# Optimization experiments

Hardware: AMD Instinct MI355X
Metric: run time of the kernel (lower is better)

The kernel has to match this reference:

```python
import jax, jax.numpy as jnp
import numpy as np

N_NODES = 50000
N_EDGES = 800000
IN_CH = 128
OUT_CH = 64
BN_EPS = 1e-5


def setup_inputs() -> dict:
    key = jax.random.key(0)
    k1, k2, k3 = jax.random.split(key, 3)
    x = jax.random.normal(k1, (N_NODES, IN_CH), dtype=jnp.float32)
    edge_index = jax.random.randint(k2, (2, N_EDGES), 0, N_NODES, dtype=jnp.int64)
    W = jax.random.normal(k3, (IN_CH, OUT_CH), dtype=jnp.float32) / np.sqrt(IN_CH)
    bias = jnp.zeros((OUT_CH,), dtype=jnp.float32)
    gamma = jnp.ones((OUT_CH,), dtype=jnp.float32)
    beta = jnp.zeros((OUT_CH,), dtype=jnp.float32)
    return {"x": x, "edge_index": edge_index, "W": W, "bias": bias,
            "gamma": gamma, "beta": beta}


def reference(x, edge_index, W, bias, gamma, beta):
    N = x.shape[0]
    # Linear transform first (GCNConv order): [N, out]
    h = x @ W
    # Add self-loops
    loops = jnp.arange(N, dtype=edge_index.dtype)
    src = jnp.concatenate([edge_index[0], loops])  # [E+N]
    dst = jnp.concatenate([edge_index[1], loops])
    # Symmetric GCN normalization: deg^{-1/2}[src] * deg^{-1/2}[dst]
    ones = jnp.ones(dst.shape[0], dtype=h.dtype)
    deg = jax.ops.segment_sum(ones, dst, num_segments=N)
    dinv = jnp.where(deg > 0, jax.lax.rsqrt(deg), 0.0)
    norm = dinv[src] * dinv[dst]  # [E+N]
    # Gather, scale, scatter-add
    msgs = h[src] * norm[:, None]  # [E+N, out]
    agg = jax.ops.segment_sum(msgs, dst, num_segments=N) + bias  # [N, out]
    # tanh activation
    a = jnp.tanh(agg)
    # BatchNorm over node dim (training mode, biased var)
    mean = jnp.mean(a, axis=0)
    var = jnp.mean(jnp.square(a - mean), axis=0)
    return gamma * (a - mean) * jax.lax.rsqrt(var + BN_EPS) + beta
```

## Files before the change

kernel.cpp:

```cpp
#include <hip/hip_runtime.h>
#include <hip/hip_bf16.h>
#include <math.h>

#define N_NODES 50000
#define N_EDGES 800000
#define IN_CH 128
#define OUT_CH 64
#define BN_EPS 1e-5f
#define CAP 64

typedef __attribute__((ext_vector_type(8))) short short8;
typedef __attribute__((ext_vector_type(4))) float f32x4;

__device__ __forceinline__ float bf16u_to_f32(uint u) { return __uint_as_float(u << 16); }

__device__ __forceinline__ ushort f32_to_bf16(float f) {
    uint u = __float_as_uint(f);
    uint r = (u + 0x7fff + ((u >> 16) & 1)) >> 16;
    return (ushort)r;
}

__global__ void fill_slots_kernel(const int4* __restrict__ esrc4, const int4* __restrict__ edst4,
                                  int* __restrict__ cnt, ushort* __restrict__ slot, int E4) {
    int i = blockIdx.x * blockDim.x + threadIdx.x;
    if (i < E4) {
        int4 s = esrc4[i];
        int4 d = edst4[i];
        int p;
        p = atomicAdd(&cnt[d.x], 1); if (p < CAP) slot[d.x * CAP + p] = (ushort)s.x;
        p = atomicAdd(&cnt[d.y], 1); if (p < CAP) slot[d.y * CAP + p] = (ushort)s.y;
        p = atomicAdd(&cnt[d.z], 1); if (p < CAP) slot[d.z * CAP + p] = (ushort)s.z;
        p = atomicAdd(&cnt[d.w], 1); if (p < CAP) slot[d.w * CAP + p] = (ushort)s.w;
    }
}

__global__ void prep_kernel(const int* __restrict__ cnt, float* __restrict__ dinv,
                            float* __restrict__ sums, int N) {
    int i = blockIdx.x * blockDim.x + threadIdx.x;
    if (i < N) dinv[i] = rsqrtf((float)(cnt[i] + 1));
    if (i < 128) sums[i] = 0.0f;
}

#define XPAD 136
__global__ __launch_bounds__(256) void gemm_mfma_kernel(const float* __restrict__ x,
                                                        const float* __restrict__ W,
                                                        ushort* __restrict__ hb, int N) {
    __shared__ ushort xs[64 * XPAD];
    __shared__ ushort wt[64 * XPAD];
    int t = threadIdx.x;
    int lane = t & 63;
    int w = t >> 6;
    int nn = lane & 15;
    int quad = lane >> 4;
    int row0 = blockIdx.x * 64;

#pragma unroll
    for (int i = 0; i < 32; ++i) {
        int wlin = t + 256 * i;
        int k = wlin >> 6, n = wlin & 63;
        wt[n * XPAD + k] = f32_to_bf16(W[wlin]);
    }
#pragma unroll
    for (int i = 0; i < 8; ++i) {
        int linear4 = t + 256 * i;
        int r = linear4 >> 5;
        int c4 = linear4 & 31;
        int gr = row0 + r; if (gr >= N) gr = N - 1;
        float4 v = *(const float4*)(x + (size_t)gr * IN_CH + c4 * 4);
        ushort u0 = f32_to_bf16(v.x), u1 = f32_to_bf16(v.y);
        ushort u2 = f32_to_bf16(v.z), u3 = f32_to_bf16(v.w);
        uint2 packed = make_uint2((uint)u0 | ((uint)u1 << 16), (uint)u2 | ((uint)u3 << 16));
        *(uint2*)&xs[r * XPAD + c4 * 4] = packed;
    }
    __syncthreads();

    short8 bfrag[4][4];
#pragma unroll
    for (int t2 = 0; t2 < 4; ++t2)
#pragma unroll
        for (int c = 0; c < 4; ++c)
            bfrag[t2][c] = *(const short8*)&wt[(16 * t2 + nn) * XPAD + 32 * c + quad * 8];

    f32x4 acc[4] = {{0.f, 0.f, 0.f, 0.f}, {0.f, 0.f, 0.f, 0.f},
                    {0.f, 0.f, 0.f, 0.f}, {0.f, 0.f, 0.f, 0.f}};
#pragma unroll
    for (int c = 0; c < 4; ++c) {
        short8 afrag = *(const short8*)&xs[(16 * w + nn) * XPAD + 32 * c + quad * 8];
#pragma unroll
        for (int t2 = 0; t2 < 4; ++t2)
            acc[t2] = __builtin_amdgcn_mfma_f32_16x16x32_bf16(afrag, bfrag[t2][c], acc[t2], 0, 0, 0);
    }

#pragma unroll
    for (int t2 = 0; t2 < 4; ++t2) {
#pragma unroll
        for (int r = 0; r < 4; ++r) {
            int row = row0 + 16 * w + quad * 4 + r;
            if (row < N) hb[(size_t)row * OUT_CH + 16 * t2 + nn] = f32_to_bf16(acc[t2][r]);
        }
    }
}

__global__ __launch_bounds__(256) void gather_fused_kernel(const int* __restrict__ cnt,
                                                           const ushort* __restrict__ slot,
                                                           const float* __restrict__ dinv,
                                                           const ushort* __restrict__ hb,
                                                           const float* __restrict__ bias,
                                                           float* __restrict__ out,
                                                           float* __restrict__ sums, int N) {
    int t = threadIdx.x;
    int lane = t & 63;
    int wid = (blockIdx.x * blockDim.x + t) >> 6;
    int nw = (gridDim.x * blockDim.x) >> 6;
    float bias_c = bias[lane];
    float ssum = 0.f, ssq = 0.f;

    for (int d = wid; d < N; d += nw) {
        float dd = dinv[d];
        float acc = bf16u_to_f32(hb[(size_t)d * OUT_CH + lane]) * dd * dd;
        int m = cnt[d]; if (m > CAP) m = CAP;
        int sv = __builtin_nontemporal_load(&slot[(size_t)d * CAP + lane]);
        if (lane >= m) sv = 0;
        float dv = dinv[sv];
        int j = 0;
        for (; j + 3 < m; j += 4) {
            int s0 = __shfl(sv, j + 0); float w0 = __shfl(dv, j + 0);
            int s1 = __shfl(sv, j + 1); float w1 = __shfl(dv, j + 1);
            int s2 = __shfl(sv, j + 2); float w2 = __shfl(dv, j + 2);
            int s3 = __shfl(sv, j + 3); float w3 = __shfl(dv, j + 3);
            uint h0 = hb[(size_t)s0 * OUT_CH + lane];
            uint h1 = hb[(size_t)s1 * OUT_CH + lane];
            uint h2 = hb[(size_t)s2 * OUT_CH + lane];
            uint h3 = hb[(size_t)s3 * OUT_CH + lane];
            acc += bf16u_to_f32(h0) * (w0 * dd);
            acc += bf16u_to_f32(h1) * (w1 * dd);
            acc += bf16u_to_f32(h2) * (w2 * dd);
            acc += bf16u_to_f32(h3) * (w3 * dd);
        }
        for (; j < m; ++j) {
            int s = __shfl(sv, j);
            float ww = __shfl(dv, j) * dd;
            acc += bf16u_to_f32(hb[(size_t)s * OUT_CH + lane]) * ww;
        }
        float v = tanhf(acc + bias_c);
        out[(size_t)d * OUT_CH + lane] = v;
        ssum += v;
        ssq += v * v;
    }

    __shared__ float ls[256];
    __shared__ float ls2[256];
    ls[t] = ssum; ls2[t] = ssq;
    __syncthreads();
    if (t < 128) { ls[t] += ls[t + 128]; ls2[t] += ls2[t + 128]; }
    __syncthreads();
    if (t < 64) {
        atomicAdd(&sums[t], ls[t] + ls[t + 64]);
        atomicAdd(&sums[64 + t], ls2[t] + ls2[t + 64]);
    }
}

__global__ __launch_bounds__(256) void bn_apply_kernel(float4* __restrict__ a,
                                                       const float* __restrict__ sums,
                                                       const float* __restrict__ gamma,
                                                       const float* __restrict__ beta, int total4) {
    int c0 = (threadIdx.x * 4) & 63;
    const float invN = 1.0f / (float)N_NODES;
    float4 scale, shift;
    {
        float m0 = sums[c0 + 0] * invN, m1 = sums[c0 + 1] * invN;
        float m2 = sums[c0 + 2] * invN, m3 = sums[c0 + 3] * invN;
        float v0 = sums[64 + c0 + 0] * invN - m0 * m0;
        float v1 = sums[64 + c0 + 1] * invN - m1 * m1;
        float v2 = sums[64 + c0 + 2] * invN - m2 * m2;
        float v3 = sums[64 + c0 + 3] * invN - m3 * m3;
        scale.x = gamma[c0 + 0] * rsqrtf(v0 + BN_EPS);
        scale.y = gamma[c0 + 1] * rsqrtf(v1 + BN_EPS);
        scale.z = gamma[c0 + 2] * rsqrtf(v2 + BN_EPS);
        scale.w = gamma[c0 + 3] * rsqrtf(v3 + BN_EPS);
        shift.x = beta[c0 + 0] - m0 * scale.x;
        shift.y = beta[c0 + 1] - m1 * scale.y;
        shift.z = beta[c0 + 2] - m2 * scale.z;
        shift.w = beta[c0 + 3] - m3 * scale.w;
    }
    int stride = gridDim.x * blockDim.x;
    for (int idx = blockIdx.x * blockDim.x + threadIdx.x; idx < total4; idx += stride) {
        float4 v = a[idx];
        v.x = v.x * scale.x + shift.x;
        v.y = v.y * scale.y + shift.y;
        v.z = v.z * scale.z + shift.z;
        v.w = v.w * scale.w + shift.w;
        a[idx] = v;
    }
}

extern "C" void kernel_launch(void* const* d_in, const int* in_sizes, int n_in,
                              void* d_out, int out_size, void* d_ws, size_t ws_size,
                              hipStream_t stream) {
    const float* x     = (const float*)d_in[0];
    const int*   eidx  = (const int*)d_in[1];
    const float* W     = (const float*)d_in[2];
    const float* bias  = (const float*)d_in[3];
    const float* gamma = (const float*)d_in[4];
    const float* beta  = (const float*)d_in[5];
    float* out = (float*)d_out;

    const int4* esrc4 = (const int4*)eidx;
    const int4* edst4 = (const int4*)(eidx + N_EDGES);

    ushort* hb   = (ushort*)d_ws;
    int*   cnt   = (int*)(hb + (size_t)N_NODES * OUT_CH);
    float* sums  = (float*)(cnt + N_NODES);
    float* dinv  = sums + 128;
    ushort* slot = (ushort*)(dinv + N_NODES);

    hipMemsetAsync(cnt, 0, (size_t)N_NODES * 4, stream);
    fill_slots_kernel<<<(N_EDGES / 4 + 255) / 256, 256, 0, stream>>>(esrc4, edst4, cnt, slot, N_EDGES / 4);
    prep_kernel<<<(N_NODES + 255) / 256, 256, 0, stream>>>(cnt, dinv, sums, N_NODES);
    gemm_mfma_kernel<<<(N_NODES + 63) / 64, 256, 0, stream>>>(x, W, hb, N_NODES);
    gather_fused_kernel<<<2048, 256, 0, stream>>>(cnt, slot, dinv, hb, bias, out, sums, N_NODES);
    bn_apply_kernel<<<512, 256, 0, stream>>>((float4*)out, sums, gamma, beta, N_NODES * OUT_CH / 4);
}
```

Baseline: 234.4 us.

## Replace fixed-capacity slot adjacency with compact count-scan-fill CSR buckets

```diff
diff --git a/kernel.cpp b/kernel.cpp
--- a/kernel.cpp
+++ b/kernel.cpp
@@ -7,7 +7,8 @@
 #define IN_CH 128
 #define OUT_CH 64
 #define BN_EPS 1e-5f
-#define CAP 64
+#define GB 782
+#define CB 782
 
 typedef __attribute__((ext_vector_type(8))) short short8;
 typedef __attribute__((ext_vector_type(4))) float f32x4;
@@ -20,34 +21,29 @@
     return (ushort)r;
 }
 
-__global__ void fill_slots_kernel(const int4* __restrict__ esrc4, const int4* __restrict__ edst4,
-                                  int* __restrict__ cnt, ushort* __restrict__ slot, int E4) {
-    int i = blockIdx.x * blockDim.x + threadIdx.x;
-    if (i < E4) {
-        int4 s = esrc4[i];
-        int4 d = edst4[i];
-        int p;
-        p = atomicAdd(&cnt[d.x], 1); if (p < CAP) slot[d.x * CAP + p] = (ushort)s.x;
-        p = atomicAdd(&cnt[d.y], 1); if (p < CAP) slot[d.y * CAP + p] = (ushort)s.y;
-        p = atomicAdd(&cnt[d.z], 1); if (p < CAP) slot[d.z * CAP + p] = (ushort)s.z;
-        p = atomicAdd(&cnt[d.w], 1); if (p < CAP) slot[d.w * CAP + p] = (ushort)s.w;
-    }
-}
-
-__global__ void prep_kernel(const int* __restrict__ cnt, float* __restrict__ dinv,
-                            float* __restrict__ sums, int N) {
-    int i = blockIdx.x * blockDim.x + threadIdx.x;
-    if (i < N) dinv[i] = rsqrtf((float)(cnt[i] + 1));
-    if (i < 128) sums[i] = 0.0f;
-}
-
 #define XPAD 136
-__global__ __launch_bounds__(256) void gemm_mfma_kernel(const float* __restrict__ x,
-                                                        const float* __restrict__ W,
-                                                        ushort* __restrict__ hb, int N) {
+
+__global__ __launch_bounds__(256) void gemm_count_kernel(const float* __restrict__ x,
+                                                         const float* __restrict__ W,
+                                                         ushort* __restrict__ hb,
+                                                         const int4* __restrict__ edst4,
+                                                         int* __restrict__ cnt, int N, int E4) {
     __shared__ ushort xs[64 * XPAD];
     __shared__ ushort wt[64 * XPAD];
     int t = threadIdx.x;
+
+    if (blockIdx.x >= GB) {
+        int i = (blockIdx.x - GB) * 256 + t;
+        if (i < E4) {
+            int4 d = edst4[i];
+            atomicAdd(&cnt[d.x], 1);
+            atomicAdd(&cnt[d.y], 1);
+            atomicAdd(&cnt[d.z], 1);
+            atomicAdd(&cnt[d.w], 1);
+        }
+        return;
+    }
+
     int lane = t & 63;
     int w = t >> 6;
     int nn = lane & 15;
@@ -101,8 +97,53 @@
     }
 }
 
+__global__ __launch_bounds__(256) void alloc_kernel(const int* __restrict__ cnt,
+                                                    int* __restrict__ gcur,
+                                                    int* __restrict__ offsets,
+                                                    int* __restrict__ cursor,
+                                                    float* __restrict__ dinv,
+                                                    float* __restrict__ sums, int N) {
+    __shared__ int ls[256];
+    __shared__ int sbase;
+    int t = threadIdx.x;
+    int i = blockIdx.x * 256 + t;
+    int c = (i < N) ? cnt[i] : 0;
+    ls[t] = c;
+    __syncthreads();
+    for (int off = 1; off < 256; off <<= 1) {
+        int u = (t >= off) ? ls[t - off] : 0;
+        __syncthreads();
+        ls[t] += u;
+        __syncthreads();
+    }
+    if (t == 255) sbase = atomicAdd(gcur, ls[255]);
+    __syncthreads();
+    if (i < N) {
+        int excl = ls[t] - c + sbase;
+        offsets[i] = excl;
+        cursor[i] = excl;
+        dinv[i] = rsqrtf((float)(c + 1));
+    }
+    if (blockIdx.x == 0 && t < 128) sums[t] = 0.0f;
+}
+
+__global__ void fill_kernel(const int4* __restrict__ esrc4, const int4* __restrict__ edst4,
+                            int* __restrict__ cursor, ushort* __restrict__ bucket, int E4) {
+    int i = blockIdx.x * blockDim.x + threadIdx.x;
+    if (i < E4) {
+        int4 s = esrc4[i];
+        int4 d = edst4[i];
+        int p;
+        p = atomicAdd(&cursor[d.x], 1); bucket[p] = (ushort)s.x;
+        p = atomicAdd(&cursor[d.y], 1); bucket[p] = (ushort)s.y;
+        p = atomicAdd(&cursor[d.z], 1); bucket[p] = (ushort)s.z;
+        p = atomicAdd(&cursor[d.w], 1); bucket[p] = (ushort)s.w;
+    }
+}
+
 __global__ __launch_bounds__(256) void gather_fused_kernel(const int* __restrict__ cnt,
-                                                           const ushort* __restrict__ slot,
+                                                           const int* __restrict__ offsets,
+                                                           const ushort* __restrict__ bucket,
                                                            const float* __restrict__ dinv,
                                                            const ushort* __restrict__ hb,
                                                            const float* __restrict__ bias,
@@ -118,29 +159,36 @@
     for (int d = wid; d < N; d += nw) {
         float dd = dinv[d];
         float acc = bf16u_to_f32(hb[(size_t)d * OUT_CH + lane]) * dd * dd;
-        int m = cnt[d]; if (m > CAP) m = CAP;
-        int sv = __builtin_nontemporal_load(&slot[(size_t)d * CAP + lane]);
-        if (lane >= m) sv = 0;
-        float dv = dinv[sv];
-        int j = 0;
-        for (; j + 3 < m; j += 4) {
-            int s0 = __shfl(sv, j + 0); float w0 = __shfl(dv, j + 0);
-            int s1 = __shfl(sv, j + 1); float w1 = __shfl(dv, j + 1);
-            int s2 = __shfl(sv, j + 2); float w2 = __shfl(dv, j + 2);
-            int s3 = __shfl(sv, j + 3); float w3 = __shfl(dv, j + 3);
-            uint h0 = hb[(size_t)s0 * OUT_CH + lane];
-            uint h1 = hb[(size_t)s1 * OUT_CH + lane];
-            uint h2 = hb[(size_t)s2 * OUT_CH + lane];
-            uint h3 = hb[(size_t)s3 * OUT_CH + lane];
-            acc += bf16u_to_f32(h0) * (w0 * dd);
-            acc += bf16u_to_f32(h1) * (w1 * dd);
-            acc += bf16u_to_f32(h2) * (w2 * dd);
-            acc += bf16u_to_f32(h3) * (w3 * dd);
-        }
-        for (; j < m; ++j) {
-            int s = __shfl(sv, j);
-            float ww = __shfl(dv, j) * dd;
-            acc += bf16u_to_f32(hb[(size_t)s * OUT_CH + lane]) * ww;
+        int b0 = offsets[d];
+        int b1 = b0 + cnt[d];
+        for (int base = b0; base < b1; base += 64) {
+            int idx = base + lane;
+            int sv = 0; float dv = 0.f;
+            if (idx < b1) {
+                sv = __builtin_nontemporal_load(&bucket[idx]);
+                dv = dinv[sv];
+            }
+            int m = b1 - base; if (m > 64) m = 64;
+            int j = 0;
+            for (; j + 3 < m; j += 4) {
+                int s0 = __shfl(sv, j + 0); float w0 = __shfl(dv, j + 0);
+                int s1 = __shfl(sv, j + 1); float w1 = __shfl(dv, j + 1);
+                int s2 = __shfl(sv, j + 2); float w2 = __shfl(dv, j + 2);
+                int s3 = __shfl(sv, j + 3); float w3 = __shfl(dv, j + 3);
+                uint h0 = hb[(size_t)s0 * OUT_CH + lane];
+                uint h1 = hb[(size_t)s1 * OUT_CH + lane];
+                uint h2 = hb[(size_t)s2 * OUT_CH + lane];
+                uint h3 = hb[(size_t)s3 * OUT_CH + lane];
+                acc += bf16u_to_f32(h0) * (w0 * dd);
+                acc += bf16u_to_f32(h1) * (w1 * dd);
+                acc += bf16u_to_f32(h2) * (w2 * dd);
+                acc += bf16u_to_f32(h3) * (w3 * dd);
+            }
+            for (; j < m; ++j) {
+                int s = __shfl(sv, j);
+                float ww = __shfl(dv, j) * dd;
+                acc += bf16u_to_f32(hb[(size_t)s * OUT_CH + lane]) * ww;
+            }
         }
         float v = tanhf(acc + bias_c);
         out[(size_t)d * OUT_CH + lane] = v;
@@ -207,17 +255,21 @@
 
     const int4* esrc4 = (const int4*)eidx;
     const int4* edst4 = (const int4*)(eidx + N_EDGES);
-
-    ushort* hb   = (ushort*)d_ws;
-    int*   cnt   = (int*)(hb + (size_t)N_NODES * OUT_CH);
-    float* sums  = (float*)(cnt + N_NODES);
-    float* dinv  = sums + 128;
-    ushort* slot = (ushort*)(dinv + N_NODES);
-
-    hipMemsetAsync(cnt, 0, (size_t)N_NODES * 4, stream);
-    fill_slots_kernel<<<(N_EDGES / 4 + 255) / 256, 256, 0, stream>>>(esrc4, edst4, cnt, slot, N_EDGES / 4);
-    prep_kernel<<<(N_NODES + 255) / 256, 256, 0, stream>>>(cnt, dinv, sums, N_NODES);
-    gemm_mfma_kernel<<<(N_NODES + 63) / 64, 256, 0, stream>>>(x, W, hb, N_NODES);
-    gather_fused_kernel<<<2048, 256, 0, stream>>>(cnt, slot, dinv, hb, bias, out, sums, N_NODES);
+    const int E4 = N_EDGES / 4;
+
+    ushort* hb    = (ushort*)d_ws;
+    int*   cnt    = (int*)(hb + (size_t)N_NODES * OUT_CH);
+    int*   gcur   = cnt + N_NODES;
+    float* sums   = (float*)(gcur + 1);
+    int*   offs   = (int*)(sums + 128);
+    int*   cursor = offs + N_NODES;
+    float* dinv   = (float*)(cursor + N_NODES);
+    ushort* bucket = (ushort*)(dinv + N_NODES);
+
+    hipMemsetAsync(cnt, 0, (size_t)(N_NODES + 1) * 4, stream);
+    gemm_count_kernel<<<GB + CB, 256, 0, stream>>>(x, W, hb, edst4, cnt, N_NODES, E4);
+    alloc_kernel<<<(N_NODES + 255) / 256, 256, 0, stream>>>(cnt, gcur, offs, cursor, dinv, sums, N_NODES);
+    fill_kernel<<<(E4 + 255) / 256, 256, 0, stream>>>(esrc4, edst4, cursor, bucket, E4);
+    gather_fused_kernel<<<2048, 256, 0, stream>>>(cnt, offs, bucket, dinv, hb, bias, out, sums, N_NODES);
     bn_apply_kernel<<<512, 256, 0, stream>>>((float4*)out, sums, gamma, beta, N_NODES * OUT_CH / 4);
 }
```

After: 258.9 us. 1.1x slower.

## Halve slot capacity with overflow list and process two nodes per wavefront

Applied to the files above, without the earlier changes.

```diff
diff --git a/kernel.cpp b/kernel.cpp
--- a/kernel.cpp
+++ b/kernel.cpp
@@ -7,7 +7,8 @@
 #define IN_CH 128
 #define OUT_CH 64
 #define BN_EPS 1e-5f
-#define CAP 64
+#define CAP 32
+#define OVF_MAX 8192
 
 typedef __attribute__((ext_vector_type(8))) short short8;
 typedef __attribute__((ext_vector_type(4))) float f32x4;
@@ -21,16 +22,25 @@
 }
 
 __global__ void fill_slots_kernel(const int4* __restrict__ esrc4, const int4* __restrict__ edst4,
-                                  int* __restrict__ cnt, ushort* __restrict__ slot, int E4) {
+                                  int* __restrict__ cnt, ushort* __restrict__ slot,
+                                  int* __restrict__ ovf_cnt, int2* __restrict__ ovf, int E4) {
     int i = blockIdx.x * blockDim.x + threadIdx.x;
     if (i < E4) {
         int4 s = esrc4[i];
         int4 d = edst4[i];
-        int p;
-        p = atomicAdd(&cnt[d.x], 1); if (p < CAP) slot[d.x * CAP + p] = (ushort)s.x;
-        p = atomicAdd(&cnt[d.y], 1); if (p < CAP) slot[d.y * CAP + p] = (ushort)s.y;
-        p = atomicAdd(&cnt[d.z], 1); if (p < CAP) slot[d.z * CAP + p] = (ushort)s.z;
-        p = atomicAdd(&cnt[d.w], 1); if (p < CAP) slot[d.w * CAP + p] = (ushort)s.w;
+        int p, q;
+        p = atomicAdd(&cnt[d.x], 1);
+        if (p < CAP) slot[d.x * CAP + p] = (ushort)s.x;
+        else { q = atomicAdd(ovf_cnt, 1); if (q < OVF_MAX) ovf[q] = make_int2(d.x, s.x); }
+        p = atomicAdd(&cnt[d.y], 1);
+        if (p < CAP) slot[d.y * CAP + p] = (ushort)s.y;
+        else { q = atomicAdd(ovf_cnt, 1); if (q < OVF_MAX) ovf[q] = make_int2(d.y, s.y); }
+        p = atomicAdd(&cnt[d.z], 1);
+        if (p < CAP) slot[d.z * CAP + p] = (ushort)s.z;
+        else { q = atomicAdd(ovf_cnt, 1); if (q < OVF_MAX) ovf[q] = make_int2(d.z, s.z); }
+        p = atomicAdd(&cnt[d.w], 1);
+        if (p < CAP) slot[d.w * CAP + p] = (ushort)s.w;
+        else { q = atomicAdd(ovf_cnt, 1); if (q < OVF_MAX) ovf[q] = make_int2(d.w, s.w); }
     }
 }
 
@@ -106,46 +116,114 @@
                                                            const float* __restrict__ dinv,
                                                            const ushort* __restrict__ hb,
                                                            const float* __restrict__ bias,
+                                                           const int* __restrict__ ovf_cnt,
+                                                           const int2* __restrict__ ovf,
                                                            float* __restrict__ out,
                                                            float* __restrict__ sums, int N) {
     int t = threadIdx.x;
     int lane = t & 63;
+    int lj = lane & 31;
+    int half = lane >> 5;
     int wid = (blockIdx.x * blockDim.x + t) >> 6;
     int nw = (gridDim.x * blockDim.x) >> 6;
     float bias_c = bias[lane];
+    int nov = *ovf_cnt; if (nov > OVF_MAX) nov = OVF_MAX;
     float ssum = 0.f, ssq = 0.f;
 
-    for (int d = wid; d < N; d += nw) {
-        float dd = dinv[d];
-        float acc = bf16u_to_f32(hb[(size_t)d * OUT_CH + lane]) * dd * dd;
-        int m = cnt[d]; if (m > CAP) m = CAP;
-        int sv = __builtin_nontemporal_load(&slot[(size_t)d * CAP + lane]);
-        if (lane >= m) sv = 0;
+    for (int d0 = wid; d0 < N; d0 += 2 * nw) {
+        int d1 = d0 + nw;
+        bool has1 = d1 < N;
+        int d1c = has1 ? d1 : d0;
+        int m0r = cnt[d0];
+        int m1r = has1 ? cnt[d1c] : 0;
+        int m0 = m0r < CAP ? m0r : CAP;
+        int m1 = m1r < CAP ? m1r : CAP;
+        float dd0 = dinv[d0];
+        float dd1 = has1 ? dinv[d1c] : 0.f;
+
+        int soff = (half == 0) ? (d0 * CAP + lj) : (d1c * CAP + lj);
+        int sv = slot[soff];
+        int mv = (half == 0) ? m0 : m1;
+        if (lj >= mv) sv = 0;
         float dv = dinv[sv];
+
+        float acc0 = bf16u_to_f32(hb[(size_t)d0 * OUT_CH + lane]) * dd0 * dd0;
+        float acc1 = has1 ? bf16u_to_f32(hb[(size_t)d1c * OUT_CH + lane]) * dd1 * dd1 : 0.f;
+
+        int mm = m0 > m1 ? m0 : m1;
         int j = 0;
-        for (; j + 3 < m; j += 4) {
-            int s0 = __shfl(sv, j + 0); float w0 = __shfl(dv, j + 0);
-            int s1 = __shfl(sv, j + 1); float w1 = __shfl(dv, j + 1);
-            int s2 = __shfl(sv, j + 2); float w2 = __shfl(dv, j + 2);
-            int s3 = __shfl(sv, j + 3); float w3 = __shfl(dv, j + 3);
-            uint h0 = hb[(size_t)s0 * OUT_CH + lane];
-            uint h1 = hb[(size_t)s1 * OUT_CH + lane];
-            uint h2 = hb[(size_t)s2 * OUT_CH + lane];
-            uint h3 = hb[(size_t)s3 * OUT_CH + lane];
-            acc += bf16u_to_f32(h0) * (w0 * dd);
-            acc += bf16u_to_f32(h1) * (w1 * dd);
-            acc += bf16u_to_f32(h2) * (w2 * dd);
-            acc += bf16u_to_f32(h3) * (w3 * dd);
-        }
-        for (; j < m; ++j) {
-            int s = __shfl(sv, j);
-            float ww = __shfl(dv, j) * dd;
-            acc += bf16u_to_f32(hb[(size_t)s * OUT_CH + lane]) * ww;
-        }
-        float v = tanhf(acc + bias_c);
-        out[(size_t)d * OUT_CH + lane] = v;
-        ssum += v;
-        ssq += v * v;
+        for (; j + 3 < mm; j += 4) {
+            int a0 = __shfl(sv, j + 0); float u0 = __shfl(dv, j + 0);
+            int a1 = __shfl(sv, j + 1); float u1 = __shfl(dv, j + 1);
+            int a2 = __shfl(sv, j + 2); float u2 = __shfl(dv, j + 2);
+            int a3 = __shfl(sv, j + 3); float u3 = __shfl(dv, j + 3);
+            int b0 = __shfl(sv, 32 + j + 0); float q0 = __shfl(dv, 32 + j + 0);
+            int b1 = __shfl(sv, 32 + j + 1); float q1 = __shfl(dv, 32 + j + 1);
+            int b2 = __shfl(sv, 32 + j + 2); float q2 = __shfl(dv, 32 + j + 2);
+            int b3 = __shfl(sv, 32 + j + 3); float q3 = __shfl(dv, 32 + j + 3);
+            uint ha0 = hb[(size_t)a0 * OUT_CH + lane];
+            uint ha1 = hb[(size_t)a1 * OUT_CH + lane];
+            uint ha2 = hb[(size_t)a2 * OUT_CH + lane];
+            uint ha3 = hb[(size_t)a3 * OUT_CH + lane];
+            uint hc0 = hb[(size_t)b0 * OUT_CH + lane];
+            uint hc1 = hb[(size_t)b1 * OUT_CH + lane];
+            uint hc2 = hb[(size_t)b2 * OUT_CH + lane];
+            uint hc3 = hb[(size_t)b3 * OUT_CH + lane];
+            float w0 = (j + 0 < m0) ? u0 * dd0 : 0.f;
+            float w1 = (j + 1 < m0) ? u1 * dd0 : 0.f;
+            float w2 = (j + 2 < m0) ? u2 * dd0 : 0.f;
+            float w3 = (j + 3 < m0) ? u3 * dd0 : 0.f;
+            float z0 = (j + 0 < m1) ? q0 * dd1 : 0.f;
+            float z1 = (j + 1 < m1) ? q1 * dd1 : 0.f;
+            float z2 = (j + 2 < m1) ? q2 * dd1 : 0.f;
+            float z3 = (j + 3 < m1) ? q3 * dd1 : 0.f;
+            acc0 += bf16u_to_f32(ha0) * w0;
+            acc0 += bf16u_to_f32(ha1) * w1;
+            acc0 += bf16u_to_f32(ha2) * w2;
+            acc0 += bf16u_to_f32(ha3) * w3;
+            acc1 += bf16u_to_f32(hc0) * z0;
+            acc1 += bf16u_to_f32(hc1) * z1;
+            acc1 += bf16u_to_f32(hc2) * z2;
+            acc1 += bf16u_to_f32(hc3) * z3;
+        }
+        for (; j < mm; ++j) {
+            int a = __shfl(sv, j); float u = __shfl(dv, j);
+            int b = __shfl(sv, 32 + j); float q = __shfl(dv, 32 + j);
+            uint ha = hb[(size_t)a * OUT_CH + lane];
+            uint hc = hb[(size_t)b * OUT_CH + lane];
+            float w = (j < m0) ? u * dd0 : 0.f;
+            float z = (j < m1) ? q * dd1 : 0.f;
+            acc0 += bf16u_to_f32(ha) * w;
+            acc1 += bf16u_to_f32(hc) * z;
+        }
+
+        if (m0r > CAP) {
+            for (int i = 0; i < nov; ++i) {
+                int2 e = ovf[i];
+                if (e.x == d0) {
+                    float ww = dinv[e.y] * dd0;
+                    acc0 += bf16u_to_f32(hb[(size_t)e.y * OUT_CH + lane]) * ww;
+                }
+            }
+        }
+        if (has1 && m1r > CAP) {
+            for (int i = 0; i < nov; ++i) {
+                int2 e = ovf[i];
+                if (e.x == d1) {
+                    float ww = dinv[e.y] * dd1;
+                    acc1 += bf16u_to_f32(hb[(size_t)e.y * OUT_CH + lane]) * ww;
+                }
+            }
+        }
+
+        float v0 = tanhf(acc0 + bias_c);
+        out[(size_t)d0 * OUT_CH + lane] = v0;
+        ssum += v0; ssq += v0 * v0;
+        if (has1) {
+            float v1 = tanhf(acc1 + bias_c);
+            out[(size_t)d1 * OUT_CH + lane] = v1;
+            ssum += v1; ssq += v1 * v1;
+        }
     }
 
     __shared__ float ls[256];
@@ -207,17 +285,20 @@
 
     const int4* esrc4 = (const int4*)eidx;
     const int4* edst4 = (const int4*)(eidx + N_EDGES);
-
-    ushort* hb   = (ushort*)d_ws;
-    int*   cnt   = (int*)(hb + (size_t)N_NODES * OUT_CH);
-    float* sums  = (float*)(cnt + N_NODES);
-    float* dinv  = sums + 128;
-    ushort* slot = (ushort*)(dinv + N_NODES);
-
-    hipMemsetAsync(cnt, 0, (size_t)N_NODES * 4, stream);
-    fill_slots_kernel<<<(N_EDGES / 4 + 255) / 256, 256, 0, stream>>>(esrc4, edst4, cnt, slot, N_EDGES / 4);
+    const int E4 = N_EDGES / 4;
+
+    ushort* hb     = (ushort*)d_ws;
+    int*    cnt    = (int*)(hb + (size_t)N_NODES * OUT_CH);
+    int*    ovfc   = cnt + N_NODES;
+    float*  sums   = (float*)(ovfc + 2);
+    float*  dinv   = sums + 128;
+    ushort* slot   = (ushort*)(dinv + N_NODES);
+    int2*   ovf    = (int2*)(slot + (size_t)N_NODES * CAP);
+
+    hipMemsetAsync(cnt, 0, (size_t)(N_NODES + 2) * 4, stream);
+    fill_slots_kernel<<<(E4 + 255) / 256, 256, 0, stream>>>(esrc4, edst4, cnt, slot, ovfc, ovf, E4);
     prep_kernel<<<(N_NODES + 255) / 256, 256, 0, stream>>>(cnt, dinv, sums, N_NODES);
     gemm_mfma_kernel<<<(N_NODES + 63) / 64, 256, 0, stream>>>(x, W, hb, N_NODES);
-    gather_fused_kernel<<<2048, 256, 0, stream>>>(cnt, slot, dinv, hb, bias, out, sums, N_NODES);
+    gather_fused_kernel<<<2048, 256, 0, stream>>>(cnt, slot, dinv, hb, bias, ovfc, ovf, out, sums, N_NODES);
     bn_apply_kernel<<<512, 256, 0, stream>>>((float4*)out, sums, gamma, beta, N_NODES * OUT_CH / 4);
 }
```

Result: slower. 255.4 us (+9.0%).
